# Kernel tuning notes

Measured on AMD Instinct MI355X. Metric: run time of the kernel, lower is better.

Reference implementation:

```python
import jax, jax.numpy as jnp
import numpy as np
from functools import partial

B, T, F = 4096, 256, 32
H1, H2, NT = 64, 32, 3


def _lstm_layer(x, W_ih, W_hh, b_ih, b_hh):
    """Torch-style LSTM (batch_first). x: [B,T,Fin], W_ih: [4H,Fin], W_hh: [4H,H].
    Gate order i, f, g, o. Returns all hidden states [B,T,H]."""
    Bsz = x.shape[0]
    H = W_hh.shape[1]
    # Precompute input contribution for all timesteps (one big GEMM)
    xg = jnp.einsum('btf,gf->btg', x, W_ih) + b_ih + b_hh  # [B,T,4H]

    def step(carry, xg_t):
        h, c = carry
        gates = xg_t + h @ W_hh.T  # [B,4H]
        i, f, g, o = jnp.split(gates, 4, axis=-1)
        i = jax.nn.sigmoid(i)
        f = jax.nn.sigmoid(f)
        g = jnp.tanh(g)
        o = jax.nn.sigmoid(o)
        c = f * c + i * g
        h = o * jnp.tanh(c)
        return (h, c), h

    init = (jnp.zeros((Bsz, H), x.dtype), jnp.zeros((Bsz, H), x.dtype))
    _, hs = jax.lax.scan(step, init, jnp.swapaxes(xg, 0, 1))  # hs: [T,B,H]
    return jnp.swapaxes(hs, 0, 1)


def setup_inputs() -> dict:
    key = jax.random.key(0)
    ks = jax.random.split(key, 12)
    s1 = 1.0 / np.sqrt(H1)
    s2 = 1.0 / np.sqrt(H2)
    u = lambda k, shape, s: jax.random.uniform(k, shape, jnp.float32, -s, s)
    return {
        'x': jax.random.normal(ks[0], (B, T, F), jnp.float32),
        'W_ih1': u(ks[1], (4 * H1, F), s1),
        'W_hh1': u(ks[2], (4 * H1, H1), s1),
        'b_ih1': u(ks[3], (4 * H1,), s1),
        'b_hh1': u(ks[4], (4 * H1,), s1),
        'W_ih2': u(ks[5], (4 * H2, H1), s2),
        'W_hh2': u(ks[6], (4 * H2, H2), s2),
        'b_ih2': u(ks[7], (4 * H2,), s2),
        'b_hh2': u(ks[8], (4 * H2,), s2),
        'W_head': u(ks[9], (NT, H2), s2),
        'b_head': u(ks[10], (NT,), s2),
    }


def reference(x, W_ih1, W_hh1, b_ih1, b_hh1, W_ih2, W_hh2, b_ih2, b_hh2, W_head, b_head):
    h1 = _lstm_layer(x, W_ih1, W_hh1, b_ih1, b_hh1)   # [B,T,64]; dropout is identity in eval
    h2 = _lstm_layer(h1, W_ih2, W_hh2, b_ih2, b_hh2)  # [B,T,32]
    last = h2[:, -1, :]                               # [B,32]
    return last @ W_head.T + b_head                   # [B,3]
```

## Files before the change

kernel.cpp:

```cpp
#include <hip/hip_runtime.h>

#define Bsz 4096
#define Tt  256
#define Ff  32
#define H1  64
#define H2  32
#define NTAPS 3
#define BT  8
#define NTHR 512
#define CH  16

typedef _Float16 half8  __attribute__((ext_vector_type(8)));
typedef __fp16   fp16x2 __attribute__((ext_vector_type(2)));
typedef float    f32x4  __attribute__((ext_vector_type(4)));

#define H1S 72
#define H2S 40
#define HDS 33

__device__ __forceinline__ float lstm_unit(float pi, float pf, float pg, float po,
                                           float& c) {
    const float K1 = 1.4426950408889634f;
    float ei = __builtin_amdgcn_exp2f(-K1 * pi);
    float ef = __builtin_amdgcn_exp2f(-K1 * pf);
    float eg = __builtin_amdgcn_exp2f(-2.0f * K1 * __builtin_fabsf(pg));
    float eo = __builtin_amdgcn_exp2f(-K1 * po);
    float f_ = __builtin_amdgcn_rcpf(1.0f + ef);
    float ig = (1.0f - eg) * __builtin_amdgcn_rcpf((1.0f + ei) * (1.0f + eg));
    ig = __builtin_copysignf(ig, pg);
    c = f_ * c + ig;
    float ec = __builtin_amdgcn_exp2f(-2.0f * K1 * __builtin_fabsf(c));
    float th = (1.0f - ec) * __builtin_amdgcn_rcpf((1.0f + eo) * (1.0f + ec));
    return __builtin_copysignf(th, c);
}

#define MFMA16(a, b, c) __builtin_amdgcn_mfma_f32_16x16x32_f16((a), (b), (c), 0, 0, 0)

__device__ __forceinline__ void dma16(const float* gp, const float* lp) {
    __builtin_amdgcn_global_load_lds(
        (const __attribute__((address_space(1))) void*)gp,
        (__attribute__((address_space(3))) void*)lp, 16, 0, 0);
}

__global__ __launch_bounds__(NTHR, 4)
void lstm2_fused(const float* __restrict__ x,
                 const float* __restrict__ Wih1, const float* __restrict__ Whh1,
                 const float* __restrict__ bih1, const float* __restrict__ bhh1,
                 const float* __restrict__ Wih2, const float* __restrict__ Whh2,
                 const float* __restrict__ bih2, const float* __restrict__ bhh2,
                 const float* __restrict__ Whead, const float* __restrict__ bhead,
                 float* __restrict__ out)
{
    __shared__ __align__(16) _Float16 sH1[2][BT][H1S];
    __shared__ __align__(16) _Float16 sH2[2][BT][H2S];
    __shared__ __align__(16) float    sXC[2][CH][8][8][4];
    __shared__ __align__(16) float    sHead[BT][HDS];

    const int tid  = threadIdx.x;
    const int wid  = tid >> 6;
    const int lane = tid & 63;
    const int l15  = lane & 15;
    const int q    = lane >> 4;
    const int row8 = l15 & 7;
    const int b0   = blockIdx.x * BT;
    const int w4   = wid & 3;
    const bool isL1 = (wid < 4);

    const int colL1 = w4 * 16 + l15;
    const int r0  = (q >> 1) * 2, r1 = r0 + 1;
    const int bLo = (q & 1) * 4 + (q >> 1) * 2;
    const int hT   = w4 >> 1, wpar = w4 & 1;
    const int hL2  = hT * 16 + l15;
    const int rL2  = 2 * wpar + (q >> 1);
    const int bL2  = (q & 1) * 4 + 2 * wpar + (q >> 1);

    const int bL  = lane & 7;
    const int f4L = lane >> 3;
    const float* gbase = x + (size_t)(b0 + bL) * Tt * Ff + f4L * 4;

    if (!isL1) {
        #pragma unroll
        for (int j = 0; j < 4; ++j) {
            int t = (w4 << 2) | j;
            dma16(gbase + (size_t)t * Ff, &sXC[0][t][0][0][0]);
        }
    }

    half8 w[4][3];
    float bias[4];
    if (isL1) {
        #pragma unroll
        for (int G = 0; G < 4; ++G) {
            int gr = G * 64 + w4 * 16 + l15;
            #pragma unroll
            for (int c = 0; c < 3; ++c) {
                half8 v;
                #pragma unroll
                for (int e = 0; e < 8; ++e) {
                    int k = c * 32 + q * 8 + e;
                    float f = (k < H1) ? Whh1[gr * H1 + k] : Wih1[gr * Ff + (k - H1)];
                    v[e] = (_Float16)f;
                }
                w[G][c] = v;
            }
            bias[G] = bih1[gr] + bhh1[gr];
        }
    } else {
        #pragma unroll
        for (int G = 0; G < 4; ++G) {
            int gr = G * 32 + hT * 16 + l15;
            #pragma unroll
            for (int c = 0; c < 3; ++c) {
                half8 v;
                #pragma unroll
                for (int e = 0; e < 8; ++e) {
                    int kk = q * 8 + e;
                    float f = (c == 0) ? Whh2[gr * H2 + kk]
                                       : Wih2[gr * H1 + (c - 1) * 32 + kk];
                    v[e] = (_Float16)f;
                }
                w[G][c] = v;
            }
            bias[G] = bih2[gr] + bhh2[gr];
        }
    }

    for (int idx = tid; idx < BT * H1S; idx += NTHR) ((_Float16*)sH1[1])[idx] = (_Float16)0.0f;
    for (int idx = tid; idx < BT * H2S; idx += NTHR) ((_Float16*)sH2[1])[idx] = (_Float16)0.0f;

    __syncthreads();

    float csA = 0.0f, csB = 0.0f;

    for (int i = 0; i <= Tt; ++i) {
        const int cur = i & 1, nxt = cur ^ 1;
        const int t16 = i & (CH - 1), cbuf = (i >> 4) & 1;

        if (!isL1 && t16 == 0 && i + CH < Tt) {
            const float* gb = gbase + (size_t)(i + CH) * Ff;
            #pragma unroll
            for (int j = 0; j < 4; ++j) {
                int t = (w4 << 2) | j;
                dma16(gb + (size_t)t * Ff, &sXC[cbuf ^ 1][t][0][0][0]);
            }
        }

        half8 a0 = *(const half8*)&sH1[nxt][row8][q * 8];
        half8 a1 = *(const half8*)&sH1[nxt][row8][32 + q * 8];

        if (isL1) {
            if (i < Tt) {
                f32x4 lo = *(const f32x4*)&sXC[cbuf][t16][2 * q][row8][0];
                f32x4 hi = *(const f32x4*)&sXC[cbuf][t16][2 * q + 1][row8][0];
                union { half8 v; fp16x2 h[4]; } axu;
                axu.h[0] = __builtin_amdgcn_cvt_pkrtz(lo[0], lo[1]);
                axu.h[1] = __builtin_amdgcn_cvt_pkrtz(lo[2], lo[3]);
                axu.h[2] = __builtin_amdgcn_cvt_pkrtz(hi[0], hi[1]);
                axu.h[3] = __builtin_amdgcn_cvt_pkrtz(hi[2], hi[3]);

                f32x4 acc[4];
                #pragma unroll
                for (int G = 0; G < 4; ++G) {
                    f32x4 a = {bias[G], bias[G], bias[G], bias[G]};
                    a = MFMA16(a0, w[G][0], a);
                    a = MFMA16(a1, w[G][1], a);
                    a = MFMA16(axu.v, w[G][2], a);
                    acc[G] = a;
                }
                float h0  = lstm_unit(acc[0][r0], acc[1][r0], acc[2][r0], acc[3][r0], csA);
                float h1v = lstm_unit(acc[0][r1], acc[1][r1], acc[2][r1], acc[3][r1], csB);
                sH1[cur][bLo][colL1]     = (_Float16)h0;
                sH1[cur][bLo + 1][colL1] = (_Float16)h1v;
            }
        } else if (i >= 1) {
            half8 ah = *(const half8*)&sH2[cur][row8][q * 8];
            f32x4 acc[4];
            #pragma unroll
            for (int G = 0; G < 4; ++G) {
                f32x4 a = {bias[G], bias[G], bias[G], bias[G]};
                a = MFMA16(ah, w[G][0], a);
                a = MFMA16(a0, w[G][1], a);
                a = MFMA16(a1, w[G][2], a);
                acc[G] = a;
            }
            float h2v = lstm_unit(acc[0][rL2], acc[1][rL2], acc[2][rL2], acc[3][rL2], csA);
            sH2[nxt][bL2][hL2] = (_Float16)h2v;
            if (i == Tt) sHead[bL2][hL2] = h2v;
        }

        __syncthreads();
    }

    if (tid < BT * NTAPS) {
        int b = tid / NTAPS, n = tid - b * NTAPS;
        float s = bhead[n];
        #pragma unroll
        for (int k = 0; k < H2; ++k) s = fmaf(sHead[b][k], Whead[n * H2 + k], s);
        out[(size_t)(b0 + b) * NTAPS + n] = s;
    }
}

extern "C" void kernel_launch(void* const* d_in, const int* in_sizes, int n_in,
                              void* d_out, int out_size, void* d_ws, size_t ws_size,
                              hipStream_t stream) {
    const float* xp    = (const float*)d_in[0];
    const float* Wih1  = (const float*)d_in[1];
    const float* Whh1  = (const float*)d_in[2];
    const float* bih1  = (const float*)d_in[3];
    const float* bhh1  = (const float*)d_in[4];
    const float* Wih2  = (const float*)d_in[5];
    const float* Whh2  = (const float*)d_in[6];
    const float* bih2  = (const float*)d_in[7];
    const float* bhh2  = (const float*)d_in[8];
    const float* Whead = (const float*)d_in[9];
    const float* bhead = (const float*)d_in[10];
    float* outp = (float*)d_out;

    hipLaunchKernelGGL(lstm2_fused, dim3(Bsz / BT), dim3(NTHR), 0, stream,
                       xp, Wih1, Whh1, bih1, bhh1, Wih2, Whh2, bih2, bhh2,
                       Whead, bhead, outp);
}
```

Before: 410.3 us.

## Double batch tile and offload layer-1 input projection to layer-2 waves

After: 392.3 us. 4.4% less time.

```diff
diff --git a/kernel.cpp b/kernel.cpp
--- a/kernel.cpp
+++ b/kernel.cpp
@@ -6,7 +6,7 @@
 #define H1  64
 #define H2  32
 #define NTAPS 3
-#define BT  8
+#define BT  16
 #define NTHR 512
 #define CH  16
 
@@ -25,10 +25,12 @@
     float ef = __builtin_amdgcn_exp2f(-K1 * pf);
     float eg = __builtin_amdgcn_exp2f(-2.0f * K1 * __builtin_fabsf(pg));
     float eo = __builtin_amdgcn_exp2f(-K1 * po);
-    float f_ = __builtin_amdgcn_rcpf(1.0f + ef);
-    float ig = (1.0f - eg) * __builtin_amdgcn_rcpf((1.0f + ei) * (1.0f + eg));
-    ig = __builtin_copysignf(ig, pg);
-    c = f_ * c + ig;
+    float p1 = (1.0f + ei) * (1.0f + eg);
+    float pf1 = 1.0f + ef;
+    float R  = __builtin_amdgcn_rcpf(p1 * pf1);
+    float t1 = c * p1;
+    float t2 = __builtin_copysignf(1.0f - eg, pg) * pf1;
+    c = (t1 + t2) * R;
     float ec = __builtin_amdgcn_exp2f(-2.0f * K1 * __builtin_fabsf(c));
     float th = (1.0f - ec) * __builtin_amdgcn_rcpf((1.0f + eo) * (1.0f + ec));
     return __builtin_copysignf(th, c);
@@ -42,7 +44,16 @@
         (__attribute__((address_space(3))) void*)lp, 16, 0, 0);
 }
 
-__global__ __launch_bounds__(NTHR, 4)
+__device__ __forceinline__ half8 cvt8(f32x4 lo, f32x4 hi) {
+    union { half8 v; fp16x2 h[4]; } ax;
+    ax.h[0] = __builtin_amdgcn_cvt_pkrtz(lo[0], lo[1]);
+    ax.h[1] = __builtin_amdgcn_cvt_pkrtz(lo[2], lo[3]);
+    ax.h[2] = __builtin_amdgcn_cvt_pkrtz(hi[0], hi[1]);
+    ax.h[3] = __builtin_amdgcn_cvt_pkrtz(hi[2], hi[3]);
+    return ax.v;
+}
+
+__global__ __launch_bounds__(NTHR, 2)
 void lstm2_fused(const float* __restrict__ x,
                  const float* __restrict__ Wih1, const float* __restrict__ Whh1,
                  const float* __restrict__ bih1, const float* __restrict__ bhh1,
@@ -53,7 +64,8 @@
 {
     __shared__ __align__(16) _Float16 sH1[2][BT][H1S];
     __shared__ __align__(16) _Float16 sH2[2][BT][H2S];
-    __shared__ __align__(16) float    sXC[2][CH][8][8][4];
+    __shared__ __align__(16) float    sXC[2][CH][8][BT][4];
+    __shared__ __align__(16) float    sXG[2][4][4][64][4];
     __shared__ __align__(16) float    sHead[BT][HDS];
 
     const int tid  = threadIdx.x;
@@ -61,67 +73,68 @@
     const int lane = tid & 63;
     const int l15  = lane & 15;
     const int q    = lane >> 4;
-    const int row8 = l15 & 7;
     const int b0   = blockIdx.x * BT;
-    const int w4   = wid & 3;
+    const int u    = wid & 3;
     const bool isL1 = (wid < 4);
 
-    const int colL1 = w4 * 16 + l15;
-    const int r0  = (q >> 1) * 2, r1 = r0 + 1;
-    const int bLo = (q & 1) * 4 + (q >> 1) * 2;
-    const int hT   = w4 >> 1, wpar = w4 & 1;
-    const int hL2  = hT * 16 + l15;
-    const int rL2  = 2 * wpar + (q >> 1);
-    const int bL2  = (q & 1) * 4 + 2 * wpar + (q >> 1);
-
-    const int bL  = lane & 7;
-    const int f4L = lane >> 3;
-    const float* gbase = x + (size_t)(b0 + bL) * Tt * Ff + f4L * 4;
+    const int hT = u & 1, rh = u >> 1;
+    const int colL1 = u * 16 + l15;
+
+    const int bL  = lane & 15;
+    const int f4b = lane >> 4;
+    const float* gbase = x + (size_t)(b0 + bL) * Tt * Ff;
 
     if (!isL1) {
         #pragma unroll
         for (int j = 0; j < 4; ++j) {
-            int t = (w4 << 2) | j;
-            dma16(gbase + (size_t)t * Ff, &sXC[0][t][0][0][0]);
-        }
-    }
-
-    half8 w[4][3];
-    float bias[4];
+            int tl = u * 4 + j;
+            #pragma unroll
+            for (int h = 0; h < 2; ++h)
+                dma16(gbase + (size_t)tl * Ff + (h * 4 + f4b) * 4,
+                      &sXC[0][tl][h * 4][0][0]);
+        }
+    }
+
+    half8 wA[4][3];
+    half8 wX[4];
+    float biasA[4], biasX[4];
     if (isL1) {
         #pragma unroll
         for (int G = 0; G < 4; ++G) {
-            int gr = G * 64 + w4 * 16 + l15;
-            #pragma unroll
-            for (int c = 0; c < 3; ++c) {
+            int gr = G * 64 + colL1;
+            #pragma unroll
+            for (int c = 0; c < 2; ++c) {
                 half8 v;
                 #pragma unroll
-                for (int e = 0; e < 8; ++e) {
-                    int k = c * 32 + q * 8 + e;
-                    float f = (k < H1) ? Whh1[gr * H1 + k] : Wih1[gr * Ff + (k - H1)];
-                    v[e] = (_Float16)f;
-                }
-                w[G][c] = v;
-            }
-            bias[G] = bih1[gr] + bhh1[gr];
+                for (int e = 0; e < 8; ++e)
+                    v[e] = (_Float16)Whh1[gr * H1 + c * 32 + q * 8 + e];
+                wA[G][c] = v;
+            }
+            wA[G][2] = wA[G][1];
+            biasA[G] = 0.0f;
+            biasX[G] = 0.0f;
         }
     } else {
         #pragma unroll
         for (int G = 0; G < 4; ++G) {
-            int gr = G * 32 + hT * 16 + l15;
-            #pragma unroll
-            for (int c = 0; c < 3; ++c) {
-                half8 v;
-                #pragma unroll
-                for (int e = 0; e < 8; ++e) {
-                    int kk = q * 8 + e;
-                    float f = (c == 0) ? Whh2[gr * H2 + kk]
-                                       : Wih2[gr * H1 + (c - 1) * 32 + kk];
-                    v[e] = (_Float16)f;
-                }
-                w[G][c] = v;
-            }
-            bias[G] = bih2[gr] + bhh2[gr];
+            int gr2 = G * 32 + hT * 16 + l15;
+            half8 v0, v1, v2, vx;
+            #pragma unroll
+            for (int e = 0; e < 8; ++e) {
+                int k = q * 8 + e;
+                v0[e] = (_Float16)Whh2[gr2 * H2 + k];
+                v1[e] = (_Float16)Wih2[gr2 * H1 + k];
+                v2[e] = (_Float16)Wih2[gr2 * H1 + 32 + k];
+            }
+            wA[G][0] = v0; wA[G][1] = v1; wA[G][2] = v2;
+            biasA[G] = bih2[gr2] + bhh2[gr2];
+
+            int grx = G * 64 + u * 16 + l15;
+            #pragma unroll
+            for (int e = 0; e < 8; ++e)
+                vx[e] = (_Float16)Wih1[grx * Ff + q * 8 + e];
+            wX[G] = vx;
+            biasX[G] = bih1[grx] + bhh1[grx];
         }
     }
 
@@ -130,64 +143,115 @@
 
     __syncthreads();
 
-    float csA = 0.0f, csB = 0.0f;
-
-    for (int i = 0; i <= Tt; ++i) {
+    if (!isL1) {
+        f32x4 lo = *(const f32x4*)&sXC[0][0][2 * q][l15][0];
+        f32x4 hi = *(const f32x4*)&sXC[0][0][2 * q + 1][l15][0];
+        half8 ax = cvt8(lo, hi);
+        #pragma unroll
+        for (int G = 0; G < 4; ++G) {
+            f32x4 a = {biasX[G], biasX[G], biasX[G], biasX[G]};
+            a = MFMA16(ax, wX[G], a);
+            *(f32x4*)&sXG[0][u][G][lane][0] = a;
+        }
+    }
+    __syncthreads();
+
+    float cs0 = 0.0f, cs1 = 0.0f, cs2 = 0.0f, cs3 = 0.0f;
+
+    #pragma unroll 2
+    for (int i = 0; i < Tt; ++i) {
         const int cur = i & 1, nxt = cur ^ 1;
-        const int t16 = i & (CH - 1), cbuf = (i >> 4) & 1;
-
-        if (!isL1 && t16 == 0 && i + CH < Tt) {
+        const int cbuf = (i >> 4) & 1;
+
+        if (!isL1 && (i & (CH - 1)) == 0 && i + CH < Tt) {
             const float* gb = gbase + (size_t)(i + CH) * Ff;
             #pragma unroll
             for (int j = 0; j < 4; ++j) {
-                int t = (w4 << 2) | j;
-                dma16(gb + (size_t)t * Ff, &sXC[cbuf ^ 1][t][0][0][0]);
-            }
-        }
-
-        half8 a0 = *(const half8*)&sH1[nxt][row8][q * 8];
-        half8 a1 = *(const half8*)&sH1[nxt][row8][32 + q * 8];
+                int tl = u * 4 + j;
+                #pragma unroll
+                for (int h = 0; h < 2; ++h)
+                    dma16(gb + (size_t)tl * Ff + (h * 4 + f4b) * 4,
+                          &sXC[cbuf ^ 1][tl][h * 4][0][0]);
+            }
+        }
+
+        half8 a0 = *(const half8*)&sH1[nxt][l15][q * 8];
+        half8 a1 = *(const half8*)&sH1[nxt][l15][32 + q * 8];
 
         if (isL1) {
-            if (i < Tt) {
-                f32x4 lo = *(const f32x4*)&sXC[cbuf][t16][2 * q][row8][0];
-                f32x4 hi = *(const f32x4*)&sXC[cbuf][t16][2 * q + 1][row8][0];
-                union { half8 v; fp16x2 h[4]; } axu;
-                axu.h[0] = __builtin_amdgcn_cvt_pkrtz(lo[0], lo[1]);
-                axu.h[1] = __builtin_amdgcn_cvt_pkrtz(lo[2], lo[3]);
-                axu.h[2] = __builtin_amdgcn_cvt_pkrtz(hi[0], hi[1]);
-                axu.h[3] = __builtin_amdgcn_cvt_pkrtz(hi[2], hi[3]);
-
+            f32x4 acc[4];
+            #pragma unroll
+            for (int G = 0; G < 4; ++G) {
+                f32x4 a = *(const f32x4*)&sXG[cur][u][G][lane][0];
+                a = MFMA16(a0, wA[G][0], a);
+                a = MFMA16(a1, wA[G][1], a);
+                acc[G] = a;
+            }
+            float h0 = lstm_unit(acc[0][0], acc[1][0], acc[2][0], acc[3][0], cs0);
+            float h1v = lstm_unit(acc[0][1], acc[1][1], acc[2][1], acc[3][1], cs1);
+            float h2v = lstm_unit(acc[0][2], acc[1][2], acc[2][2], acc[3][2], cs2);
+            float h3v = lstm_unit(acc[0][3], acc[1][3], acc[2][3], acc[3][3], cs3);
+            sH1[cur][q * 4 + 0][colL1] = (_Float16)h0;
+            sH1[cur][q * 4 + 1][colL1] = (_Float16)h1v;
+            sH1[cur][q * 4 + 2][colL1] = (_Float16)h2v;
+            sH1[cur][q * 4 + 3][colL1] = (_Float16)h3v;
+        } else {
+            if (i >= 1) {
+                half8 ah = *(const half8*)&sH2[cur][l15][q * 8];
                 f32x4 acc[4];
                 #pragma unroll
                 for (int G = 0; G < 4; ++G) {
-                    f32x4 a = {bias[G], bias[G], bias[G], bias[G]};
-                    a = MFMA16(a0, w[G][0], a);
-                    a = MFMA16(a1, w[G][1], a);
-                    a = MFMA16(axu.v, w[G][2], a);
+                    f32x4 a = {biasA[G], biasA[G], biasA[G], biasA[G]};
+                    a = MFMA16(ah, wA[G][0], a);
+                    a = MFMA16(a0, wA[G][1], a);
+                    a = MFMA16(a1, wA[G][2], a);
                     acc[G] = a;
                 }
-                float h0  = lstm_unit(acc[0][r0], acc[1][r0], acc[2][r0], acc[3][r0], csA);
-                float h1v = lstm_unit(acc[0][r1], acc[1][r1], acc[2][r1], acc[3][r1], csB);
-                sH1[cur][bLo][colL1]     = (_Float16)h0;
-                sH1[cur][bLo + 1][colL1] = (_Float16)h1v;
-            }
-        } else if (i >= 1) {
-            half8 ah = *(const half8*)&sH2[cur][row8][q * 8];
+                int r = rh * 2;
+                float hA = lstm_unit(acc[0][r],     acc[1][r],     acc[2][r],     acc[3][r],     cs0);
+                float hB = lstm_unit(acc[0][r + 1], acc[1][r + 1], acc[2][r + 1], acc[3][r + 1], cs1);
+                sH2[nxt][q * 4 + r][hT * 16 + l15]     = (_Float16)hA;
+                sH2[nxt][q * 4 + r + 1][hT * 16 + l15] = (_Float16)hB;
+            }
+            if (i + 1 < Tt) {
+                const int t = i + 1, cb = (t >> 4) & 1, t16 = t & (CH - 1);
+                f32x4 lo = *(const f32x4*)&sXC[cb][t16][2 * q][l15][0];
+                f32x4 hi = *(const f32x4*)&sXC[cb][t16][2 * q + 1][l15][0];
+                half8 ax = cvt8(lo, hi);
+                #pragma unroll
+                for (int G = 0; G < 4; ++G) {
+                    f32x4 a = {biasX[G], biasX[G], biasX[G], biasX[G]};
+                    a = MFMA16(ax, wX[G], a);
+                    *(f32x4*)&sXG[nxt][u][G][lane][0] = a;
+                }
+            }
+        }
+
+        __syncthreads();
+    }
+
+    {
+        const int cur = Tt & 1;
+        const int nxt = cur ^ 1;
+        if (!isL1) {
+            half8 a0 = *(const half8*)&sH1[nxt][l15][q * 8];
+            half8 a1 = *(const half8*)&sH1[nxt][l15][32 + q * 8];
+            half8 ah = *(const half8*)&sH2[cur][l15][q * 8];
             f32x4 acc[4];
             #pragma unroll
             for (int G = 0; G < 4; ++G) {
-                f32x4 a = {bias[G], bias[G], bias[G], bias[G]};
-                a = MFMA16(ah, w[G][0], a);
-                a = MFMA16(a0, w[G][1], a);
-                a = MFMA16(a1, w[G][2], a);
+                f32x4 a = {biasA[G], biasA[G], biasA[G], biasA[G]};
+                a = MFMA16(ah, wA[G][0], a);
+                a = MFMA16(a0, wA[G][1], a);
+                a = MFMA16(a1, wA[G][2], a);
                 acc[G] = a;
             }
-            float h2v = lstm_unit(acc[0][rL2], acc[1][rL2], acc[2][rL2], acc[3][rL2], csA);
-            sH2[nxt][bL2][hL2] = (_Float16)h2v;
-            if (i == Tt) sHead[bL2][hL2] = h2v;
-        }
-
+            int r = rh * 2;
+            float hA = lstm_unit(acc[0][r],     acc[1][r],     acc[2][r],     acc[3][r],     cs0);
+            float hB = lstm_unit(acc[0][r + 1], acc[1][r + 1], acc[2][r + 1], acc[3][r + 1], cs1);
+            sHead[q * 4 + r][hT * 16 + l15]     = hA;
+            sHead[q * 4 + r + 1][hT * 16 + l15] = hB;
+        }
         __syncthreads();
     }
 
```
